# Kernel optimization log

Hardware: AMD Instinct MI355X
Metric: run time of the kernel (lower is better)

Reference implementation:

```python
import jax, jax.numpy as jnp
import numpy as np

NUM_HEADS = 12
EPS = 1e-4


def setup_inputs() -> dict:
    key = jax.random.key(0)
    k1, k2, k3 = jax.random.split(key, 3)
    C = 768
    B, N = 128, 196  # B = b * num_frames = 8 * 16
    x = jax.random.normal(k1, (B, N, C), dtype=jnp.float32)
    W_qkv = jax.random.normal(k2, (3 * C, C), dtype=jnp.float32) * 0.02
    W_proj = jax.random.normal(k3, (C, C), dtype=jnp.float32) * 0.02
    b_proj = jnp.zeros((C,), dtype=jnp.float32)
    return {"x": x, "W_qkv": W_qkv, "W_proj": W_proj, "b_proj": b_proj,
            "num_frames": 16}


def reference(x, W_qkv, W_proj, b_proj, num_frames):
    B, N, C = x.shape
    h = NUM_HEADS
    e = C // h
    # qkv projection (no bias), split k-first then heads: 'b n (k h e)'
    qkv = (x @ W_qkv.T).reshape(B, N, 3, h, e)
    q, k, v = qkv[:, :, 0], qkv[:, :, 1], qkv[:, :, 2]  # [B, N, h, e]
    q_ = jax.nn.relu(q)
    k_ = jax.nn.relu(k)
    # fold frames into the sequence: (b f) n -> b (f n)
    b = B // num_frames
    S = num_frames * N
    q_ = q_.reshape(b, S, h, e)
    k_ = k_.reshape(b, S, h, e)
    v_ = v.reshape(b, S, h, e)
    # kv trick: kv[b,h,e,d] = sum_s k[b,s,h,e] v[b,s,h,d]
    kv = jnp.einsum('bshe,bshd->bhed', k_, v_)
    k_sum = k_.sum(axis=1)  # [b, h, e]
    z = 1.0 / (jnp.einsum('bshe,bhe->bsh', q_, k_sum) + EPS)  # [b, S, h]
    out = jnp.einsum('bshe,bhed->bshd', q_, kv) * z[..., None]  # [b, S, h, e]
    out = out.reshape(B, N, C)
    # output projection (dropouts are identity at eval)
    return out @ W_proj.T + b_proj
```

## Files before the change

### kernel.cpp

```cpp
#include <hip/hip_runtime.h>
#include <hip/hip_bf16.h>

#define EPS_Z 1e-4f

typedef __attribute__((ext_vector_type(8))) short bf16x8;
typedef __attribute__((ext_vector_type(4))) float f32x4;

__device__ __forceinline__ float b2f(short s) {
    union { unsigned u; float f; } cv;
    cv.u = ((unsigned)(unsigned short)s) << 16;
    return cv.f;
}

__device__ __forceinline__ void gld_lds16(const __hip_bfloat16* g, __hip_bfloat16* l) {
    __builtin_amdgcn_global_load_lds(
        (__attribute__((address_space(1))) void*)(g),
        (__attribute__((address_space(3))) void*)(l),
        16, 0, 0);
}

__global__ __launch_bounds__(256)
void cvt_f32_bf16(const float* __restrict__ in, __hip_bfloat16* __restrict__ out, int n4)
{
    int i = blockIdx.x * 256 + threadIdx.x;
    if (i >= n4) return;
    float4 v = ((const float4*)in)[i];
    union { short4 s; __hip_bfloat16 h[4]; } o;
    o.h[0] = __float2bfloat16(v.x);
    o.h[1] = __float2bfloat16(v.y);
    o.h[2] = __float2bfloat16(v.z);
    o.h[3] = __float2bfloat16(v.w);
    ((short4*)out)[i] = o.s;
}

template<int MODE, typename CT>
__global__ __launch_bounds__(256, 2)
void gemm_bt(const __hip_bfloat16* __restrict__ A,
             const __hip_bfloat16* __restrict__ B,
             CT* __restrict__ C,
             const float* __restrict__ bias,
             int K, int N, int gx)
{
    __shared__ __align__(16) __hip_bfloat16 As[128 * 64];
    __shared__ __align__(16) __hip_bfloat16 Bs[128 * 64];
    const int g = blockIdx.x;
    const int gp = (g & 7) * ((int)gridDim.x >> 3) + (g >> 3);
    const int bx = gp % gx;
    const int by = gp / gx;

    const int tid = threadIdx.x;
    const int w = tid >> 6;
    const int l = tid & 63;
    const int wr = (w >> 1) * 64;
    const int wc = (w & 1) * 64;
    const int l15 = l & 15;
    const int lq = l >> 4;
    const int rx = l15 & 7;

    f32x4 acc[4][4] = {};

    const int srow8 = l >> 3;
    const int scol = (((l & 7) ^ (l >> 3)) << 3);

    const __hip_bfloat16* Ab = A + (size_t)by * 128 * K;
    const __hip_bfloat16* Bb = B + (size_t)bx * 128 * K;

    for (int k0 = 0; k0 < K; k0 += 64) {
        __syncthreads();
        #pragma unroll
        for (int i = 0; i < 4; ++i) {
            const int chunk = w * 4 + i;
            const int row = chunk * 8 + srow8;
            gld_lds16(Ab + (size_t)row * K + (k0 + scol), As + chunk * 512);
            gld_lds16(Bb + (size_t)row * K + (k0 + scol), Bs + chunk * 512);
        }
        __syncthreads();
        #pragma unroll
        for (int kk = 0; kk < 64; kk += 32) {
            const int kb = (kk >> 3) + lq;
            const int col = (kb ^ rx) << 3;
            bf16x8 a[4], b[4];
            #pragma unroll
            for (int i = 0; i < 4; ++i)
                a[i] = *(const bf16x8*)(As + (wr + i * 16 + l15) * 64 + col);
            #pragma unroll
            for (int j = 0; j < 4; ++j)
                b[j] = *(const bf16x8*)(Bs + (wc + j * 16 + l15) * 64 + col);
            #pragma unroll
            for (int i = 0; i < 4; ++i)
                #pragma unroll
                for (int j = 0; j < 4; ++j)
                    acc[i][j] = __builtin_amdgcn_mfma_f32_16x16x32_bf16(a[i], b[j], acc[i][j], 0, 0, 0);
        }
    }

    const int crow0 = by * 128 + wr + lq * 4;
    const int ccol0 = bx * 128 + wc + l15;
    #pragma unroll
    for (int i = 0; i < 4; ++i) {
        #pragma unroll
        for (int j = 0; j < 4; ++j) {
            const int gc = ccol0 + j * 16;
            const float badd = (MODE == 2) ? bias[gc] : 0.0f;
            #pragma unroll
            for (int r = 0; r < 4; ++r) {
                const int gr = crow0 + i * 16 + r;
                float v = acc[i][j][r];
                if (MODE == 1 && gc < 1536) v = fmaxf(v, 0.0f);
                if (MODE == 2) v += badd;
                if (MODE == 1)
                    ((__hip_bfloat16*)C)[(size_t)gr * N + gc] = __float2bfloat16(v);
                else
                    ((float*)C)[(size_t)gr * N + gc] = v;
            }
        }
    }
}

__global__ __launch_bounds__(256)
void kv_mfma_kernel(const __hip_bfloat16* __restrict__ qkv,
                    float* __restrict__ kvp, float* __restrict__ ksump)
{
    const int SPLIT = 7;
    const int bh = blockIdx.x / SPLIT;
    const int ck = blockIdx.x % SPLIT;
    const int b = bh / 12, h = bh % 12;

    __shared__ __align__(16) __hip_bfloat16 kT[64 * 40];
    __shared__ __align__(16) __hip_bfloat16 vT[64 * 40];

    const int tid = threadIdx.x;
    const int w = tid >> 6, l = tid & 63;
    const int l15 = l & 15, lq = l >> 4;

    const int half = tid >> 7;
    const int idx  = tid & 127;
    const int e0 = (idx >> 4) * 8;
    const int sp = idx & 15;

    const size_t rowbase = (size_t)b * 3136 * 2304 + (half ? 1536 : 768) + h * 64 + e0;
    __hip_bfloat16* Tdst = half ? vT : kT;

    f32x4 acc[4] = {};
    f32x4 accks = {};

    bf16x8 ones;
    #pragma unroll
    for (int i = 0; i < 8; ++i) ones[i] = (short)0x3F80;

    const int s_begin = ck * 448;
    for (int s0 = s_begin; s0 < s_begin + 448; s0 += 32) {
        __syncthreads();
        bf16x8 r0 = *(const bf16x8*)(qkv + rowbase + (size_t)(s0 + 2 * sp) * 2304);
        bf16x8 r1 = *(const bf16x8*)(qkv + rowbase + (size_t)(s0 + 2 * sp + 1) * 2304);
        #pragma unroll
        for (int qq = 0; qq < 8; ++qq) {
            unsigned pk = ((unsigned)(unsigned short)r0[qq]) |
                          (((unsigned)(unsigned short)r1[qq]) << 16);
            *(unsigned*)(Tdst + (e0 + qq) * 40 + 2 * sp) = pk;
        }
        __syncthreads();
        bf16x8 a = *(const bf16x8*)(vT + (w * 16 + l15) * 40 + lq * 8);
        bf16x8 bfr[4];
        #pragma unroll
        for (int j = 0; j < 4; ++j)
            bfr[j] = *(const bf16x8*)(kT + (j * 16 + l15) * 40 + lq * 8);
        #pragma unroll
        for (int j = 0; j < 4; ++j)
            acc[j] = __builtin_amdgcn_mfma_f32_16x16x32_bf16(a, bfr[j], acc[j], 0, 0, 0);
        accks = __builtin_amdgcn_mfma_f32_16x16x32_bf16(ones, bfr[w], accks, 0, 0, 0);
    }

    float* kvdst = kvp + ((size_t)(bh * SPLIT + ck) << 12);
    #pragma unroll
    for (int j = 0; j < 4; ++j) {
        const int col = j * 16 + l15;
        #pragma unroll
        for (int r = 0; r < 4; ++r) {
            const int row = w * 16 + lq * 4 + r;
            kvdst[row * 64 + col] = acc[j][r];
        }
    }
    if (lq == 0)
        ksump[(size_t)(bh * SPLIT + ck) * 64 + w * 16 + l15] = accks[0];
}

__global__ __launch_bounds__(256)
void kv_reduce(const float* __restrict__ kvp, const float* __restrict__ ksump,
               __hip_bfloat16* __restrict__ kvb, float* __restrict__ ksum)
{
    const int SPLIT = 7;
    const int bh = blockIdx.x;
    const int tid = threadIdx.x;

    const float* base = kvp + ((size_t)bh * SPLIT << 12) + tid * 16;
    float4 s0 = {}, s1 = {}, s2 = {}, s3 = {};
    #pragma unroll
    for (int p = 0; p < SPLIT; ++p) {
        const float* bp = base + ((size_t)p << 12);
        float4 a0 = *(const float4*)(bp + 0);
        float4 a1 = *(const float4*)(bp + 4);
        float4 a2 = *(const float4*)(bp + 8);
        float4 a3 = *(const float4*)(bp + 12);
        s0.x += a0.x; s0.y += a0.y; s0.z += a0.z; s0.w += a0.w;
        s1.x += a1.x; s1.y += a1.y; s1.z += a1.z; s1.w += a1.w;
        s2.x += a2.x; s2.y += a2.y; s2.z += a2.z; s2.w += a2.w;
        s3.x += a3.x; s3.y += a3.y; s3.z += a3.z; s3.w += a3.w;
    }
    union { bf16x8 v; __hip_bfloat16 h[8]; } o0, o1;
    o0.h[0] = __float2bfloat16(s0.x); o0.h[1] = __float2bfloat16(s0.y);
    o0.h[2] = __float2bfloat16(s0.z); o0.h[3] = __float2bfloat16(s0.w);
    o0.h[4] = __float2bfloat16(s1.x); o0.h[5] = __float2bfloat16(s1.y);
    o0.h[6] = __float2bfloat16(s1.z); o0.h[7] = __float2bfloat16(s1.w);
    o1.h[0] = __float2bfloat16(s2.x); o1.h[1] = __float2bfloat16(s2.y);
    o1.h[2] = __float2bfloat16(s2.z); o1.h[3] = __float2bfloat16(s2.w);
    o1.h[4] = __float2bfloat16(s3.x); o1.h[5] = __float2bfloat16(s3.y);
    o1.h[6] = __float2bfloat16(s3.z); o1.h[7] = __float2bfloat16(s3.w);
    __hip_bfloat16* dst = kvb + ((size_t)bh << 12) + tid * 16;
    *(bf16x8*)(dst + 0) = o0.v;
    *(bf16x8*)(dst + 8) = o1.v;

    if (tid < 64) {
        float t = 0.0f;
        #pragma unroll
        for (int p = 0; p < SPLIT; ++p)
            t += ksump[(size_t)(bh * SPLIT + p) * 64 + tid];
        ksum[(size_t)bh * 64 + tid] = t;
    }
}

__global__ __launch_bounds__(256)
void attn_mfma2(const __hip_bfloat16* __restrict__ qkv,
                const __hip_bfloat16* __restrict__ kvb,
                const float* __restrict__ ksumg,
                __hip_bfloat16* __restrict__ att)
{
    const int bh = blockIdx.x / 49;
    const int mt = blockIdx.x % 49;
    const int b = bh / 12, h = bh % 12;
    const int tid = threadIdx.x;
    const int w = tid >> 6, l = tid & 63;
    const int l15 = l & 15, lq = l >> 4;

    const size_t m0 = (size_t)b * 3136 + (size_t)mt * 64 + w * 16;

    const __hip_bfloat16* qrow = qkv + (m0 + l15) * 2304 + h * 64;
    bf16x8 aq0 = *(const bf16x8*)(qrow + lq * 8);
    bf16x8 aq1 = *(const bf16x8*)(qrow + 32 + lq * 8);

    const float* ks = ksumg + (bh << 6);
    float kse[8], kse1[8];
    *(float4*)(kse)      = *(const float4*)(ks + lq * 8);
    *(float4*)(kse + 4)  = *(const float4*)(ks + lq * 8 + 4);
    *(float4*)(kse1)     = *(const float4*)(ks + 32 + lq * 8);
    *(float4*)(kse1 + 4) = *(const float4*)(ks + 32 + lq * 8 + 4);
    float zp = 0.0f;
    #pragma unroll
    for (int j = 0; j < 8; ++j)
        zp += b2f(aq0[j]) * kse[j] + b2f(aq1[j]) * kse1[j];
    zp += __shfl_xor(zp, 16);
    zp += __shfl_xor(zp, 32);
    const float zr = 1.0f / (zp + EPS_Z);

    const __hip_bfloat16* kvh = kvb + ((size_t)bh << 12);
    f32x4 acc[4] = {};
    #pragma unroll
    for (int j = 0; j < 4; ++j) {
        bf16x8 b0 = *(const bf16x8*)(kvh + (j * 16 + l15) * 64 + lq * 8);
        bf16x8 b1 = *(const bf16x8*)(kvh + (j * 16 + l15) * 64 + 32 + lq * 8);
        acc[j] = __builtin_amdgcn_mfma_f32_16x16x32_bf16(aq0, b0, acc[j], 0, 0, 0);
        acc[j] = __builtin_amdgcn_mfma_f32_16x16x32_bf16(aq1, b1, acc[j], 0, 0, 0);
    }

    float zrow[4];
    #pragma unroll
    for (int r = 0; r < 4; ++r) zrow[r] = __shfl(zr, lq * 4 + r);

    #pragma unroll
    for (int j = 0; j < 4; ++j) {
        const int col = j * 16 + l15;
        #pragma unroll
        for (int r = 0; r < 4; ++r) {
            const int row = lq * 4 + r;
            att[(m0 + row) * 768 + h * 64 + col] = __float2bfloat16(acc[j][r] * zrow[r]);
        }
    }
}

extern "C" void kernel_launch(void* const* d_in, const int* in_sizes, int n_in,
                              void* d_out, int out_size, void* d_ws, size_t ws_size,
                              hipStream_t stream)
{
    const float* x      = (const float*)d_in[0];
    const float* W_qkv  = (const float*)d_in[1];
    const float* W_proj = (const float*)d_in[2];
    const float* b_proj = (const float*)d_in[3];
    float* out = (float*)d_out;

    const int M = 25088, K = 768, N1 = 2304, N2 = 768;
    const int SPLIT = 7;

    __hip_bfloat16* qkv = (__hip_bfloat16*)d_ws;
    __hip_bfloat16* xb  = qkv + (size_t)M * N1;
    __hip_bfloat16* wqb = xb + (size_t)M * K;
    __hip_bfloat16* wpb = wqb + (size_t)N1 * K;
    float* kvp   = (float*)(wpb + (size_t)N2 * K);
    float* ksump = kvp + (size_t)SPLIT * 96 * 4096;
    float* ksum  = ksump + (size_t)SPLIT * 96 * 64;
    __hip_bfloat16* kvb = (__hip_bfloat16*)(ksum + 96 * 64);
    __hip_bfloat16* att = xb;

    cvt_f32_bf16<<<(M * K / 4 + 255) / 256, 256, 0, stream>>>(x, xb, M * K / 4);
    cvt_f32_bf16<<<(N1 * K / 4 + 255) / 256, 256, 0, stream>>>(W_qkv, wqb, N1 * K / 4);
    cvt_f32_bf16<<<(N2 * K / 4 + 255) / 256, 256, 0, stream>>>(W_proj, wpb, N2 * K / 4);

    gemm_bt<1, __hip_bfloat16><<<(M / 128) * (N1 / 128), 256, 0, stream>>>(
        xb, wqb, qkv, nullptr, K, N1, N1 / 128);
    kv_mfma_kernel<<<96 * SPLIT, 256, 0, stream>>>(qkv, kvp, ksump);
    kv_reduce<<<96, 256, 0, stream>>>(kvp, ksump, kvb, ksum);
    attn_mfma2<<<96 * 49, 256, 0, stream>>>(qkv, kvb, ksum, att);
    gemm_bt<2, float><<<(M / 128) * (N2 / 128), 256, 0, stream>>>(
        att, wpb, out, b_proj, K, N2, N2 / 128);
}
```

Before: 349.9 us.

## Fuse conversions, prefetch kv loads, reuse kv tile in attention, raise GEMM occupancy

Merges the three fp32-to-bf16 conversion launches into one kernel and raises the GEMM launch-bounds minimum to three blocks per CU. The kv accumulation kernel now prefetches the next chunk's global loads into registers during the MFMA step. The attention kernel processes two row tiles per block, loading the kv fragments once per block. The higher occupancy hint may force register spills in the GEMM, and halving the attention grid reduces parallelism.

New measurement: 336.2 us. 1.04x faster.

```diff
diff --git a/kernel.cpp b/kernel.cpp
--- a/kernel.cpp
+++ b/kernel.cpp
@@ -20,21 +20,33 @@
 }
 
 __global__ __launch_bounds__(256)
-void cvt_f32_bf16(const float* __restrict__ in, __hip_bfloat16* __restrict__ out, int n4)
-{
+void cvt_all(const float* __restrict__ x, const float* __restrict__ wq,
+             const float* __restrict__ wp,
+             __hip_bfloat16* __restrict__ xb, __hip_bfloat16* __restrict__ wqb,
+             __hip_bfloat16* __restrict__ wpb)
+{
+    const int N4X = 25088 * 768 / 4;
+    const int N4Q = 2304 * 768 / 4;
+    const int N4P = 768 * 768 / 4;
     int i = blockIdx.x * 256 + threadIdx.x;
-    if (i >= n4) return;
-    float4 v = ((const float4*)in)[i];
+    const float* src;
+    __hip_bfloat16* dst;
+    int idx;
+    if (i < N4X)            { src = x;  dst = xb;  idx = i; }
+    else if (i < N4X + N4Q) { src = wq; dst = wqb; idx = i - N4X; }
+    else if (i < N4X + N4Q + N4P) { src = wp; dst = wpb; idx = i - N4X - N4Q; }
+    else return;
+    float4 v = ((const float4*)src)[idx];
     union { short4 s; __hip_bfloat16 h[4]; } o;
     o.h[0] = __float2bfloat16(v.x);
     o.h[1] = __float2bfloat16(v.y);
     o.h[2] = __float2bfloat16(v.z);
     o.h[3] = __float2bfloat16(v.w);
-    ((short4*)out)[i] = o.s;
+    ((short4*)dst)[idx] = o.s;
 }
 
 template<int MODE, typename CT>
-__global__ __launch_bounds__(256, 2)
+__global__ __launch_bounds__(256, 3)
 void gemm_bt(const __hip_bfloat16* __restrict__ A,
              const __hip_bfloat16* __restrict__ B,
              CT* __restrict__ C,
@@ -149,10 +161,13 @@
     for (int i = 0; i < 8; ++i) ones[i] = (short)0x3F80;
 
     const int s_begin = ck * 448;
-    for (int s0 = s_begin; s0 < s_begin + 448; s0 += 32) {
+    const int s_end = s_begin + 448;
+
+    bf16x8 r0 = *(const bf16x8*)(qkv + rowbase + (size_t)(s_begin + 2 * sp) * 2304);
+    bf16x8 r1 = *(const bf16x8*)(qkv + rowbase + (size_t)(s_begin + 2 * sp + 1) * 2304);
+
+    for (int s0 = s_begin; s0 < s_end; s0 += 32) {
         __syncthreads();
-        bf16x8 r0 = *(const bf16x8*)(qkv + rowbase + (size_t)(s0 + 2 * sp) * 2304);
-        bf16x8 r1 = *(const bf16x8*)(qkv + rowbase + (size_t)(s0 + 2 * sp + 1) * 2304);
         #pragma unroll
         for (int qq = 0; qq < 8; ++qq) {
             unsigned pk = ((unsigned)(unsigned short)r0[qq]) |
@@ -160,6 +175,10 @@
             *(unsigned*)(Tdst + (e0 + qq) * 40 + 2 * sp) = pk;
         }
         __syncthreads();
+        if (s0 + 32 < s_end) {
+            r0 = *(const bf16x8*)(qkv + rowbase + (size_t)(s0 + 32 + 2 * sp) * 2304);
+            r1 = *(const bf16x8*)(qkv + rowbase + (size_t)(s0 + 33 + 2 * sp) * 2304);
+        }
         bf16x8 a = *(const bf16x8*)(vT + (w * 16 + l15) * 40 + lq * 8);
         bf16x8 bfr[4];
         #pragma unroll
@@ -235,54 +254,64 @@
                 const float* __restrict__ ksumg,
                 __hip_bfloat16* __restrict__ att)
 {
-    const int bh = blockIdx.x / 49;
-    const int mt = blockIdx.x % 49;
+    const int bh = blockIdx.x / 25;
+    const int u  = blockIdx.x % 25;
     const int b = bh / 12, h = bh % 12;
     const int tid = threadIdx.x;
     const int w = tid >> 6, l = tid & 63;
     const int l15 = l & 15, lq = l >> 4;
 
-    const size_t m0 = (size_t)b * 3136 + (size_t)mt * 64 + w * 16;
-
-    const __hip_bfloat16* qrow = qkv + (m0 + l15) * 2304 + h * 64;
-    bf16x8 aq0 = *(const bf16x8*)(qrow + lq * 8);
-    bf16x8 aq1 = *(const bf16x8*)(qrow + 32 + lq * 8);
-
+    const __hip_bfloat16* kvh = kvb + ((size_t)bh << 12);
+    bf16x8 b0[4], b1[4];
+    #pragma unroll
+    for (int j = 0; j < 4; ++j) {
+        b0[j] = *(const bf16x8*)(kvh + (j * 16 + l15) * 64 + lq * 8);
+        b1[j] = *(const bf16x8*)(kvh + (j * 16 + l15) * 64 + 32 + lq * 8);
+    }
     const float* ks = ksumg + (bh << 6);
     float kse[8], kse1[8];
     *(float4*)(kse)      = *(const float4*)(ks + lq * 8);
     *(float4*)(kse + 4)  = *(const float4*)(ks + lq * 8 + 4);
     *(float4*)(kse1)     = *(const float4*)(ks + 32 + lq * 8);
     *(float4*)(kse1 + 4) = *(const float4*)(ks + 32 + lq * 8 + 4);
-    float zp = 0.0f;
-    #pragma unroll
-    for (int j = 0; j < 8; ++j)
-        zp += b2f(aq0[j]) * kse[j] + b2f(aq1[j]) * kse1[j];
-    zp += __shfl_xor(zp, 16);
-    zp += __shfl_xor(zp, 32);
-    const float zr = 1.0f / (zp + EPS_Z);
-
-    const __hip_bfloat16* kvh = kvb + ((size_t)bh << 12);
-    f32x4 acc[4] = {};
-    #pragma unroll
-    for (int j = 0; j < 4; ++j) {
-        bf16x8 b0 = *(const bf16x8*)(kvh + (j * 16 + l15) * 64 + lq * 8);
-        bf16x8 b1 = *(const bf16x8*)(kvh + (j * 16 + l15) * 64 + 32 + lq * 8);
-        acc[j] = __builtin_amdgcn_mfma_f32_16x16x32_bf16(aq0, b0, acc[j], 0, 0, 0);
-        acc[j] = __builtin_amdgcn_mfma_f32_16x16x32_bf16(aq1, b1, acc[j], 0, 0, 0);
-    }
-
-    float zrow[4];
-    #pragma unroll
-    for (int r = 0; r < 4; ++r) zrow[r] = __shfl(zr, lq * 4 + r);
-
-    #pragma unroll
-    for (int j = 0; j < 4; ++j) {
-        const int col = j * 16 + l15;
-        #pragma unroll
-        for (int r = 0; r < 4; ++r) {
-            const int row = lq * 4 + r;
-            att[(m0 + row) * 768 + h * 64 + col] = __float2bfloat16(acc[j][r] * zrow[r]);
+
+    #pragma unroll
+    for (int t = 0; t < 2; ++t) {
+        const int mt = u * 2 + t;
+        if (mt >= 49) break;
+        const size_t m0 = (size_t)b * 3136 + (size_t)mt * 64 + w * 16;
+
+        const __hip_bfloat16* qrow = qkv + (m0 + l15) * 2304 + h * 64;
+        bf16x8 aq0 = *(const bf16x8*)(qrow + lq * 8);
+        bf16x8 aq1 = *(const bf16x8*)(qrow + 32 + lq * 8);
+
+        float zp = 0.0f;
+        #pragma unroll
+        for (int j = 0; j < 8; ++j)
+            zp += b2f(aq0[j]) * kse[j] + b2f(aq1[j]) * kse1[j];
+        zp += __shfl_xor(zp, 16);
+        zp += __shfl_xor(zp, 32);
+        const float zr = 1.0f / (zp + EPS_Z);
+
+        f32x4 acc[4] = {};
+        #pragma unroll
+        for (int j = 0; j < 4; ++j) {
+            acc[j] = __builtin_amdgcn_mfma_f32_16x16x32_bf16(aq0, b0[j], acc[j], 0, 0, 0);
+            acc[j] = __builtin_amdgcn_mfma_f32_16x16x32_bf16(aq1, b1[j], acc[j], 0, 0, 0);
+        }
+
+        float zrow[4];
+        #pragma unroll
+        for (int r = 0; r < 4; ++r) zrow[r] = __shfl(zr, lq * 4 + r);
+
+        #pragma unroll
+        for (int j = 0; j < 4; ++j) {
+            const int col = j * 16 + l15;
+            #pragma unroll
+            for (int r = 0; r < 4; ++r) {
+                const int row = lq * 4 + r;
+                att[(m0 + row) * 768 + h * 64 + col] = __float2bfloat16(acc[j][r] * zrow[r]);
+            }
         }
     }
 }
@@ -310,15 +339,14 @@
     __hip_bfloat16* kvb = (__hip_bfloat16*)(ksum + 96 * 64);
     __hip_bfloat16* att = xb;
 
-    cvt_f32_bf16<<<(M * K / 4 + 255) / 256, 256, 0, stream>>>(x, xb, M * K / 4);
-    cvt_f32_bf16<<<(N1 * K / 4 + 255) / 256, 256, 0, stream>>>(W_qkv, wqb, N1 * K / 4);
-    cvt_f32_bf16<<<(N2 * K / 4 + 255) / 256, 256, 0, stream>>>(W_proj, wpb, N2 * K / 4);
+    const int CVT_TOT = (M * K + N1 * K + N2 * K) / 4;
+    cvt_all<<<(CVT_TOT + 255) / 256, 256, 0, stream>>>(x, W_qkv, W_proj, xb, wqb, wpb);
 
     gemm_bt<1, __hip_bfloat16><<<(M / 128) * (N1 / 128), 256, 0, stream>>>(
         xb, wqb, qkv, nullptr, K, N1, N1 / 128);
     kv_mfma_kernel<<<96 * SPLIT, 256, 0, stream>>>(qkv, kvp, ksump);
     kv_reduce<<<96, 256, 0, stream>>>(kvp, ksump, kvb, ksum);
-    attn_mfma2<<<96 * 49, 256, 0, stream>>>(qkv, kvb, ksum, att);
+    attn_mfma2<<<96 * 25, 256, 0, stream>>>(qkv, kvb, ksum, att);
     gemm_bt<2, float><<<(M / 128) * (N2 / 128), 256, 0, stream>>>(
         att, wpb, out, b_proj, K, N2, N2 / 128);
 }
```
